# Kernel optimization log

Measured on AMD Instinct MI355X. Metric: run time of the kernel, lower is better.

The kernel has to match this reference:

```python
import jax, jax.numpy as jnp
import numpy as np


def setup_inputs() -> dict:
    key = jax.random.key(0)
    k0, k1, k2, k3 = jax.random.split(key, 4)
    B, in_dim, n_vars, out_dim, E = 64, 512, 512, 720, 8
    x = jax.random.normal(k0, (B, in_dim, n_vars), dtype=jnp.float32)
    # Gating: nn.Linear(in_dim, E, bias=False) -> weight [E, in_dim]
    Wg = jax.random.normal(k1, (E, in_dim), dtype=jnp.float32) * 0.02
    # Experts: nn.Linear(in_dim, out_dim) -> weight [out_dim, in_dim], bias [out_dim]
    We = jax.random.normal(k2, (E, out_dim, in_dim), dtype=jnp.float32) * 0.02
    be = jax.random.normal(k3, (E, out_dim), dtype=jnp.float32) * 0.02
    return {"x": x, "Wg": Wg, "We": We, "be": be, "top_k": 2}


def reference(x, Wg, We, be, top_k):
    # x: [B, in_len, n_vars] -> tokens along n_vars with feature dim in_len
    xt = jnp.swapaxes(x, 1, 2)                      # [B, V, D]
    gate = jax.nn.softmax(xt @ Wg.T, axis=-1)       # [B, V, E]
    weights, sel = jax.lax.top_k(gate, top_k)       # [B, V, k]
    E, O, D = We.shape
    out = jnp.zeros(xt.shape[:2] + (O,), dtype=xt.dtype)  # [B, V, O]
    for e in range(E):
        # combine weight for expert e: sum over top-k slots routed to e
        coef = jnp.sum(jnp.where(sel == e, weights, jnp.zeros_like(weights)), axis=-1)  # [B, V]
        out = out + coef[..., None] * (jnp.einsum('bvd,od->bvo', xt, We[e]) + be[e])
    return jnp.swapaxes(out, 1, 2)                  # [B, pred_len, n_vars]
```

## Files before the change

kernel.cpp:

```cpp
#include <hip/hip_runtime.h>
#include <hip/hip_bf16.h>

#define DID 512
#define NV  512
#define NB  64
#define OD  720
#define OPAD 768
#define NE  8
#define NTOK (NB * NV)
#define MAXTILE 512

typedef short  bf16x8 __attribute__((ext_vector_type(8)));
typedef float  f32x4  __attribute__((ext_vector_type(4)));

#define XT_OFF    0u
#define WB_OFF    33554432u
#define PID_OFF   39845888u
#define C1D_OFF   39976960u
#define C2D_OFF   40108032u
#define TL_OFF    40239104u
#define CL1_OFF   40370176u
#define CL2_OFF   40501248u
#define BCNT_OFF  40632320u
#define BFILL_OFF 40632576u
#define BOFF_OFF  40632832u
#define TPID_OFF  40633088u
#define TT0_OFF   40635136u
#define TEND_OFF  40637184u
#define NT_OFF    40639232u
#define SCR_OFF   40639488u
#define SCR_END   87825408u

static __device__ __forceinline__ ushort f2bf(float f) {
  unsigned u = __float_as_uint(f);
  unsigned r = (u + 0x7fffu + ((u >> 16) & 1u)) >> 16;
  return (ushort)r;
}
static __device__ __forceinline__ float bf2f(ushort u) {
  return __uint_as_float(((unsigned)u) << 16);
}
static __device__ __forceinline__ void async16(const ushort* g, ushort* l) {
  __builtin_amdgcn_global_load_lds((__attribute__((address_space(1))) void*)(g),
                                   (__attribute__((address_space(3))) void*)(l),
                                   16, 0, 0);
}
static __device__ __forceinline__ int swz(int r) { return (r & 3) ^ ((r >> 2) & 1); }

__global__ __launch_bounds__(256) void k_transpose(const float* __restrict__ x,
                                                   ushort* __restrict__ xt) {
  __shared__ float s[32][33];
  const int b  = blockIdx.z;
  const int v0 = blockIdx.x * 32;
  const int d0 = blockIdx.y * 32;
  const int tx = threadIdx.x & 31;
  const int ty = threadIdx.x >> 5;
  const float* xp = x + ((size_t)b * DID + d0 + ty) * NV + v0 + tx;
#pragma unroll
  for (int i = 0; i < 4; ++i) s[ty + i * 8][tx] = xp[(size_t)i * 8 * NV];
  __syncthreads();
#pragma unroll
  for (int i = 0; i < 4; ++i) {
    int vl = ty + i * 8;
    xt[((size_t)b * NV + v0 + vl) * DID + d0 + tx] = f2bf(s[tx][vl]);
  }
}

__global__ __launch_bounds__(256) void k_wbconv(const float* __restrict__ We,
                                                ushort* __restrict__ wb) {
  const int e = blockIdx.y;
  const int i = blockIdx.x * 256 + threadIdx.x;
  const int o = i >> 9;
  ushort val = 0;
  if (o < OD) val = f2bf(We[(size_t)e * OD * DID + i]);
  wb[(size_t)e * OPAD * DID + i] = val;
}

__global__ __launch_bounds__(256) void k_gate(const float* __restrict__ x,
                                              const float* __restrict__ Wg,
                                              int* __restrict__ pairid,
                                              float* __restrict__ c1d,
                                              float* __restrict__ c2d,
                                              int* __restrict__ bcnt) {
  __shared__ float wg[NE * DID];
  __shared__ int cnt64[64];
  const int tid = threadIdx.x;
  for (int i = tid; i < NE * DID; i += 256) wg[i] = Wg[i];
  if (tid < 64) cnt64[tid] = 0;
  __syncthreads();

  const int b = blockIdx.y;
  const int v = blockIdx.x * 256 + tid;
  const float* xp = x + (size_t)b * DID * NV + v;

  float acc[NE];
#pragma unroll
  for (int e = 0; e < NE; ++e) acc[e] = 0.f;
  for (int d = 0; d < DID; d += 4) {
    float x0 = xp[(size_t)(d + 0) * NV];
    float x1 = xp[(size_t)(d + 1) * NV];
    float x2 = xp[(size_t)(d + 2) * NV];
    float x3 = xp[(size_t)(d + 3) * NV];
#pragma unroll
    for (int e = 0; e < NE; ++e) {
      float4 w4 = *(const float4*)&wg[e * DID + d];
      acc[e] += x0 * w4.x + x1 * w4.y + x2 * w4.z + x3 * w4.w;
    }
  }
  float mx = acc[0];
#pragma unroll
  for (int e = 1; e < NE; ++e) mx = fmaxf(mx, acc[e]);
  float sum = 0.f;
#pragma unroll
  for (int e = 0; e < NE; ++e) { acc[e] = __expf(acc[e] - mx); sum += acc[e]; }
  const float inv = 1.f / sum;

  int i1 = 0; float g1 = acc[0];
#pragma unroll
  for (int e = 1; e < NE; ++e) if (acc[e] > g1) { g1 = acc[e]; i1 = e; }
  int i2 = -1; float g2 = -1.f;
#pragma unroll
  for (int e = 0; e < NE; ++e) if (e != i1 && acc[e] > g2) { g2 = acc[e]; i2 = e; }
  g1 *= inv; g2 *= inv;

  int ea, eb; float ca, cb;
  if (i1 < i2) { ea = i1; eb = i2; ca = g1; cb = g2; }
  else         { ea = i2; eb = i1; ca = g2; cb = g1; }
  const int pid = ea * 8 + eb;
  const int t = b * NV + v;
  pairid[t] = pid; c1d[t] = ca; c2d[t] = cb;
  atomicAdd(&cnt64[pid], 1);
  __syncthreads();
  if (tid < 64 && cnt64[tid]) atomicAdd(&bcnt[tid], cnt64[tid]);
}

__global__ void k_prefix(const int* __restrict__ bcnt, int* __restrict__ boffs,
                         int* __restrict__ tpid, int* __restrict__ tt0,
                         int* __restrict__ tend, int* __restrict__ ntp) {
  if (threadIdx.x != 0) return;
  int off = 0, nt = 0;
  for (int p = 0; p < 64; ++p) {
    boffs[p] = off;
    const int c = bcnt[p];
    const int end = off + c;
    for (int i = 0; i * 128 < c; ++i) {
      tpid[nt] = p; tt0[nt] = off + i * 128; tend[nt] = end; ++nt;
    }
    off = end;
  }
  ntp[0] = nt;
}

__global__ __launch_bounds__(256) void k_scatter(const int* __restrict__ pairid,
                                                 const float* __restrict__ c1d,
                                                 const float* __restrict__ c2d,
                                                 const int* __restrict__ boffs,
                                                 int* __restrict__ bfill,
                                                 int* __restrict__ tlist,
                                                 float* __restrict__ cl1,
                                                 float* __restrict__ cl2) {
  __shared__ int cnt64[64], base64[64];
  const int tid = threadIdx.x;
  if (tid < 64) cnt64[tid] = 0;
  __syncthreads();
  const int t = blockIdx.x * 256 + tid;
  const int pid = pairid[t];
  const int p = atomicAdd(&cnt64[pid], 1);
  __syncthreads();
  if (tid < 64) base64[tid] = cnt64[tid] ? atomicAdd(&bfill[tid], cnt64[tid]) : 0;
  __syncthreads();
  const int slot = boffs[pid] + base64[pid] + p;
  tlist[slot] = t; cl1[slot] = c1d[t]; cl2[slot] = c2d[t];
}

__global__ __launch_bounds__(256, 2) void k_gemm(
    const ushort* __restrict__ xt, const ushort* __restrict__ wb,
    const float* __restrict__ be, const int* __restrict__ tlist,
    const float* __restrict__ cl1, const float* __restrict__ cl2,
    const int* __restrict__ tpid, const int* __restrict__ tt0,
    const int* __restrict__ tendarr, const int* __restrict__ ntp,
    ushort* __restrict__ scratch, float* __restrict__ out, int mode) {
  const int tile = blockIdx.x;
  if (tile >= ntp[0]) return;
  const int pid  = tpid[tile];
  const int t0   = tt0[tile];
  const int tend = tendarr[tile];
  const int e1 = pid >> 3, e2 = pid & 7;
  const int o0 = blockIdx.y * 128;

  __shared__ __align__(16) ushort As[2][4096];
  __shared__ __align__(16) ushort Bs[2][4096];

  const int tid  = threadIdx.x;
  const int lane = tid & 63;
  const int w    = tid >> 6;

  const int f0 = w * 128 + lane, f1 = f0 + 64;
  const int r0 = f0 >> 2, p0 = f0 & 3, q0 = p0 ^ swz(r0);
  const int r1 = f1 >> 2, p1 = f1 & 3, q1 = p1 ^ swz(r1);

  const int aoff0 = (o0 + r0) * DID + q0 * 8;
  const int aoff1 = (o0 + r1) * DID + q1 * 8;
  const int sl0 = t0 + r0, sl1 = t0 + r1;
  const int tok0 = (sl0 < tend) ? tlist[sl0] : 0;
  const int tok1 = (sl1 < tend) ? tlist[sl1] : 0;
  const int boff0 = tok0 * DID + q0 * 8;
  const int boff1 = tok1 * DID + q1 * 8;
  const int dA0 = w * 1024, dA1 = w * 1024 + 512;

  const int m    = lane & 15;
  const int quad = lane >> 4;
  const int wo   = (w >> 1) * 64;
  const int wt   = (w & 1) * 64;

  f32x4 acc[4][4];
#pragma unroll
  for (int i = 0; i < 4; ++i)
#pragma unroll
    for (int j = 0; j < 4; ++j) acc[i][j] = (f32x4){0.f, 0.f, 0.f, 0.f};

  {
    const ushort* wA = wb + (size_t)e1 * OPAD * DID;
    async16(wA + aoff0, &As[0][dA0]);
    async16(wA + aoff1, &As[0][dA1]);
    async16(xt + boff0, &Bs[0][dA0]);
    async16(xt + boff1, &Bs[0][dA1]);
  }

  for (int kk = 0; kk < 32; ++kk) {
    __syncthreads();

    if (kk == 16) {
      float ratio[4];
#pragma unroll
      for (int j = 0; j < 4; ++j) {
        const int sl = t0 + wt + j * 16 + m;
        const bool g = sl < tend;
        const float cc1 = g ? cl1[sl] : 0.f;
        const float cc2 = g ? cl2[sl] : 1.f;
        ratio[j] = cc1 / cc2;
      }
      const float* be1p = be + e1 * OD;
#pragma unroll
      for (int i = 0; i < 4; ++i) {
        const int ob = o0 + wo + i * 16 + quad * 4;
        float b0 = 0, b1 = 0, b2 = 0, b3 = 0;
        if (ob < OD) { b0 = be1p[ob]; b1 = be1p[ob + 1]; b2 = be1p[ob + 2]; b3 = be1p[ob + 3]; }
#pragma unroll
        for (int j = 0; j < 4; ++j) {
          acc[i][j][0] = (acc[i][j][0] + b0) * ratio[j];
          acc[i][j][1] = (acc[i][j][1] + b1) * ratio[j];
          acc[i][j][2] = (acc[i][j][2] + b2) * ratio[j];
          acc[i][j][3] = (acc[i][j][3] + b3) * ratio[j];
        }
      }
    }

    const int nk = kk + 1;
    if (nk < 32) {
      const int nb = nk & 1;
      const int eA = (nk < 16) ? e1 : e2;
      const int k0 = (nk & 15) * 32;
      const ushort* wA = wb + (size_t)eA * OPAD * DID + k0;
      async16(wA + aoff0, &As[nb][dA0]);
      async16(wA + aoff1, &As[nb][dA1]);
      async16(xt + boff0 + k0, &Bs[nb][dA0]);
      async16(xt + boff1 + k0, &Bs[nb][dA1]);
    }

    const int cb = kk & 1;
    bf16x8 af[4], bfr[4];
#pragma unroll
    for (int i = 0; i < 4; ++i) {
      const int R = wo + i * 16 + m;
      af[i] = *(const bf16x8*)(&As[cb][R * 32 + ((quad ^ swz(R)) << 3)]);
    }
#pragma unroll
    for (int j = 0; j < 4; ++j) {
      const int R = wt + j * 16 + m;
      bfr[j] = *(const bf16x8*)(&Bs[cb][R * 32 + ((quad ^ swz(R)) << 3)]);
    }
#pragma unroll
    for (int i = 0; i < 4; ++i)
#pragma unroll
      for (int j = 0; j < 4; ++j)
        acc[i][j] = __builtin_amdgcn_mfma_f32_16x16x32_bf16(af[i], bfr[j],
                                                            acc[i][j], 0, 0, 0);
  }

  float c2v[4]; int tokv[4]; bool gv[4];
#pragma unroll
  for (int j = 0; j < 4; ++j) {
    const int sl = t0 + wt + j * 16 + m;
    gv[j] = sl < tend;
    c2v[j]  = gv[j] ? cl2[sl] : 0.f;
    tokv[j] = gv[j] ? tlist[sl] : 0;
  }
  const float* be2p = be + e2 * OD;
#pragma unroll
  for (int i = 0; i < 4; ++i) {
    const int ob = o0 + wo + i * 16 + quad * 4;
    if (ob < OD) {
      const float b0 = be2p[ob], b1 = be2p[ob + 1], b2 = be2p[ob + 2], b3 = be2p[ob + 3];
#pragma unroll
      for (int j = 0; j < 4; ++j) {
        if (gv[j]) {
          const float v0 = c2v[j] * (acc[i][j][0] + b0);
          const float v1 = c2v[j] * (acc[i][j][1] + b1);
          const float v2 = c2v[j] * (acc[i][j][2] + b2);
          const float v3 = c2v[j] * (acc[i][j][3] + b3);
          if (mode == 0) {
            ushort4 pk = make_ushort4(f2bf(v0), f2bf(v1), f2bf(v2), f2bf(v3));
            *(ushort4*)(scratch + (size_t)tokv[j] * OD + ob) = pk;
          } else {
            const int bb = tokv[j] >> 9, vv = tokv[j] & 511;
            float* op = out + ((size_t)bb * OD + ob) * NV + vv;
            op[0] = v0; op[(size_t)NV] = v1; op[2 * (size_t)NV] = v2; op[3 * (size_t)NV] = v3;
          }
        }
      }
    }
  }
}

__global__ __launch_bounds__(256) void k_combine(const ushort* __restrict__ scratch,
                                                 float* __restrict__ out) {
  __shared__ ushort s[64][68];
  const int v0 = blockIdx.x * 64;
  const int o0 = blockIdx.y * 64;
  const int b  = blockIdx.z;
  const int tid = threadIdx.x;
#pragma unroll
  for (int it = 0; it < 2; ++it) {
    const int c = it * 256 + tid;
    const int row = c >> 3, cg = c & 7;
    const int o = o0 + cg * 8;
    if (o + 8 <= OD) {
      const ushort* src = scratch + ((size_t)(b * NV + v0 + row)) * OD + o;
      ushort4 ua = *(const ushort4*)(src);
      ushort4 ub = *(const ushort4*)(src + 4);
      *(ushort4*)&s[row][cg * 8] = ua;
      *(ushort4*)&s[row][cg * 8 + 4] = ub;
    }
  }
  __syncthreads();
  const int vv = tid & 63;
  const int og = tid >> 6;
#pragma unroll
  for (int oi = 0; oi < 8; ++oi) {
    const int ol = (og * 8 + oi) * 2;
    const int o = o0 + ol;
    if (o < OD) {
      ushort2 u = *(const ushort2*)&s[vv][ol];
      float* op = out + ((size_t)b * OD + o) * NV + v0 + vv;
      op[0]  = bf2f(u.x);
      op[NV] = bf2f(u.y);
    }
  }
}

extern "C" void kernel_launch(void* const* d_in, const int* in_sizes, int n_in,
                              void* d_out, int out_size, void* d_ws, size_t ws_size,
                              hipStream_t stream) {
  const float* x  = (const float*)d_in[0];
  const float* Wg = (const float*)d_in[1];
  const float* We = (const float*)d_in[2];
  const float* be = (const float*)d_in[3];
  float* out = (float*)d_out;

  char* ws = (char*)d_ws;
  ushort* xt     = (ushort*)(ws + XT_OFF);
  ushort* wb     = (ushort*)(ws + WB_OFF);
  int*    pairid = (int*)   (ws + PID_OFF);
  float*  c1d    = (float*) (ws + C1D_OFF);
  float*  c2d    = (float*) (ws + C2D_OFF);
  int*    tlist  = (int*)   (ws + TL_OFF);
  float*  cl1    = (float*) (ws + CL1_OFF);
  float*  cl2    = (float*) (ws + CL2_OFF);
  int*    bcnt   = (int*)   (ws + BCNT_OFF);
  int*    bfill  = (int*)   (ws + BFILL_OFF);
  int*    boffs  = (int*)   (ws + BOFF_OFF);
  int*    tpid   = (int*)   (ws + TPID_OFF);
  int*    tt0    = (int*)   (ws + TT0_OFF);
  int*    tend   = (int*)   (ws + TEND_OFF);
  int*    ntp    = (int*)   (ws + NT_OFF);
  ushort* scratch= (ushort*)(ws + SCR_OFF);

  const int mode = (ws_size >= (size_t)SCR_END) ? 0 : 1;

  (void)hipMemsetAsync(bcnt, 0, 512, stream);

  k_transpose<<<dim3(NV / 32, DID / 32, NB), 256, 0, stream>>>(x, xt);
  k_wbconv<<<dim3(OPAD * DID / 256, NE), 256, 0, stream>>>(We, wb);
  k_gate<<<dim3(NV / 256, NB), 256, 0, stream>>>(x, Wg, pairid, c1d, c2d, bcnt);
  k_prefix<<<1, 64, 0, stream>>>(bcnt, boffs, tpid, tt0, tend, ntp);
  k_scatter<<<NTOK / 256, 256, 0, stream>>>(pairid, c1d, c2d, boffs, bfill,
                                            tlist, cl1, cl2);
  k_gemm<<<dim3(320, OPAD / 128), 256, 0, stream>>>(xt, wb, be, tlist, cl1, cl2,
                                                    tpid, tt0, tend, ntp,
                                                    scratch, out, mode);
  if (mode == 0)
    k_combine<<<dim3(NV / 64, (OD + 63) / 64, NB), 256, 0, stream>>>(scratch, out);
}
```

Baseline: 341.0 us.

## Fuse transpose/bf16 conversion into gating kernel and parallelize prefix scan

Merges the separate transpose-to-bf16 kernel and the gating kernel into one kernel, so x (64 MB fp32) is read from global memory once instead of twice. Each block handles 64 tokens with 8 waves splitting the feature dimension, then reduces partial gate logits in shared memory before softmax/top-2. Also replaces the single-thread serial prefix over expert pairs with a 64-lane wavefront shuffle scan. The trade-off is more shared memory per block and fewer, larger blocks. The transposed writes are now 16-byte per-lane stores strided by the row length, which may coalesce less well than the old LDS-tiled transpose.

Measured after the change: 322.1 us. 5.5% less time.

```diff
diff --git a/kernel.cpp b/kernel.cpp
--- a/kernel.cpp
+++ b/kernel.cpp
@@ -46,23 +46,92 @@
 }
 static __device__ __forceinline__ int swz(int r) { return (r & 3) ^ ((r >> 2) & 1); }
 
-__global__ __launch_bounds__(256) void k_transpose(const float* __restrict__ x,
-                                                   ushort* __restrict__ xt) {
-  __shared__ float s[32][33];
-  const int b  = blockIdx.z;
-  const int v0 = blockIdx.x * 32;
-  const int d0 = blockIdx.y * 32;
-  const int tx = threadIdx.x & 31;
-  const int ty = threadIdx.x >> 5;
-  const float* xp = x + ((size_t)b * DID + d0 + ty) * NV + v0 + tx;
-#pragma unroll
-  for (int i = 0; i < 4; ++i) s[ty + i * 8][tx] = xp[(size_t)i * 8 * NV];
-  __syncthreads();
-#pragma unroll
-  for (int i = 0; i < 4; ++i) {
-    int vl = ty + i * 8;
-    xt[((size_t)b * NV + v0 + vl) * DID + d0 + tx] = f2bf(s[tx][vl]);
-  }
+__global__ __launch_bounds__(512) void k_gatet(const float* __restrict__ x,
+                                               const float* __restrict__ Wg,
+                                               ushort* __restrict__ xt,
+                                               int* __restrict__ pairid,
+                                               float* __restrict__ c1d,
+                                               float* __restrict__ c2d,
+                                               int* __restrict__ bcnt) {
+  __shared__ float wg[NE * DID];
+  __shared__ float part[8][64][NE + 1];
+  __shared__ int cnt64[64];
+  const int tid = threadIdx.x;
+  for (int i = tid; i < NE * DID / 4; i += 512)
+    ((float4*)wg)[i] = ((const float4*)Wg)[i];
+  if (tid < 64) cnt64[tid] = 0;
+  __syncthreads();
+
+  const int b    = blockIdx.y;
+  const int v0   = blockIdx.x * 64;
+  const int w    = tid >> 6;
+  const int lane = tid & 63;
+  const int v    = v0 + lane;
+  const int d0   = w * 64;
+  const float* xp = x + ((size_t)b * DID + d0) * NV + v;
+  ushort* xtp = xt + ((size_t)b * NV + v) * DID + d0;
+
+  float acc[NE];
+#pragma unroll
+  for (int e = 0; e < NE; ++e) acc[e] = 0.f;
+
+  for (int c = 0; c < 64; c += 8) {
+    float xv[8];
+#pragma unroll
+    for (int u = 0; u < 8; ++u) xv[u] = xp[(size_t)(c + u) * NV];
+#pragma unroll
+    for (int e = 0; e < NE; ++e) {
+      const float* wp = &wg[e * DID + d0 + c];
+      float4 wa = *(const float4*)wp;
+      float4 wb4 = *(const float4*)(wp + 4);
+      acc[e] += xv[0] * wa.x + xv[1] * wa.y + xv[2] * wa.z + xv[3] * wa.w
+              + xv[4] * wb4.x + xv[5] * wb4.y + xv[6] * wb4.z + xv[7] * wb4.w;
+    }
+    bf16x8 pk;
+#pragma unroll
+    for (int u = 0; u < 8; ++u) pk[u] = (short)f2bf(xv[u]);
+    *(bf16x8*)(xtp + c) = pk;
+  }
+
+#pragma unroll
+  for (int e = 0; e < NE; ++e) part[w][lane][e] = acc[e];
+  __syncthreads();
+
+  if (tid < 64) {
+    float a[NE];
+#pragma unroll
+    for (int e = 0; e < NE; ++e) {
+      float s = part[0][tid][e];
+#pragma unroll
+      for (int q = 1; q < 8; ++q) s += part[q][tid][e];
+      a[e] = s;
+    }
+    float mx = a[0];
+#pragma unroll
+    for (int e = 1; e < NE; ++e) mx = fmaxf(mx, a[e]);
+    float sum = 0.f;
+#pragma unroll
+    for (int e = 0; e < NE; ++e) { a[e] = __expf(a[e] - mx); sum += a[e]; }
+    const float inv = 1.f / sum;
+
+    int i1 = 0; float g1 = a[0];
+#pragma unroll
+    for (int e = 1; e < NE; ++e) if (a[e] > g1) { g1 = a[e]; i1 = e; }
+    int i2 = -1; float g2 = -1.f;
+#pragma unroll
+    for (int e = 0; e < NE; ++e) if (e != i1 && a[e] > g2) { g2 = a[e]; i2 = e; }
+    g1 *= inv; g2 *= inv;
+
+    int ea, eb; float ca, cb;
+    if (i1 < i2) { ea = i1; eb = i2; ca = g1; cb = g2; }
+    else         { ea = i2; eb = i1; ca = g2; cb = g1; }
+    const int pid = ea * 8 + eb;
+    const int t = b * NV + v0 + tid;
+    pairid[t] = pid; c1d[t] = ca; c2d[t] = cb;
+    atomicAdd(&cnt64[pid], 1);
+  }
+  __syncthreads();
+  if (tid < 64 && cnt64[tid]) atomicAdd(&bcnt[tid], cnt64[tid]);
 }
 
 __global__ __launch_bounds__(256) void k_wbconv(const float* __restrict__ We,
@@ -75,79 +144,33 @@
   wb[(size_t)e * OPAD * DID + i] = val;
 }
 
-__global__ __launch_bounds__(256) void k_gate(const float* __restrict__ x,
-                                              const float* __restrict__ Wg,
-                                              int* __restrict__ pairid,
-                                              float* __restrict__ c1d,
-                                              float* __restrict__ c2d,
-                                              int* __restrict__ bcnt) {
-  __shared__ float wg[NE * DID];
-  __shared__ int cnt64[64];
-  const int tid = threadIdx.x;
-  for (int i = tid; i < NE * DID; i += 256) wg[i] = Wg[i];
-  if (tid < 64) cnt64[tid] = 0;
-  __syncthreads();
-
-  const int b = blockIdx.y;
-  const int v = blockIdx.x * 256 + tid;
-  const float* xp = x + (size_t)b * DID * NV + v;
-
-  float acc[NE];
-#pragma unroll
-  for (int e = 0; e < NE; ++e) acc[e] = 0.f;
-  for (int d = 0; d < DID; d += 4) {
-    float x0 = xp[(size_t)(d + 0) * NV];
-    float x1 = xp[(size_t)(d + 1) * NV];
-    float x2 = xp[(size_t)(d + 2) * NV];
-    float x3 = xp[(size_t)(d + 3) * NV];
-#pragma unroll
-    for (int e = 0; e < NE; ++e) {
-      float4 w4 = *(const float4*)&wg[e * DID + d];
-      acc[e] += x0 * w4.x + x1 * w4.y + x2 * w4.z + x3 * w4.w;
-    }
-  }
-  float mx = acc[0];
-#pragma unroll
-  for (int e = 1; e < NE; ++e) mx = fmaxf(mx, acc[e]);
-  float sum = 0.f;
-#pragma unroll
-  for (int e = 0; e < NE; ++e) { acc[e] = __expf(acc[e] - mx); sum += acc[e]; }
-  const float inv = 1.f / sum;
-
-  int i1 = 0; float g1 = acc[0];
-#pragma unroll
-  for (int e = 1; e < NE; ++e) if (acc[e] > g1) { g1 = acc[e]; i1 = e; }
-  int i2 = -1; float g2 = -1.f;
-#pragma unroll
-  for (int e = 0; e < NE; ++e) if (e != i1 && acc[e] > g2) { g2 = acc[e]; i2 = e; }
-  g1 *= inv; g2 *= inv;
-
-  int ea, eb; float ca, cb;
-  if (i1 < i2) { ea = i1; eb = i2; ca = g1; cb = g2; }
-  else         { ea = i2; eb = i1; ca = g2; cb = g1; }
-  const int pid = ea * 8 + eb;
-  const int t = b * NV + v;
-  pairid[t] = pid; c1d[t] = ca; c2d[t] = cb;
-  atomicAdd(&cnt64[pid], 1);
-  __syncthreads();
-  if (tid < 64 && cnt64[tid]) atomicAdd(&bcnt[tid], cnt64[tid]);
-}
-
 __global__ void k_prefix(const int* __restrict__ bcnt, int* __restrict__ boffs,
                          int* __restrict__ tpid, int* __restrict__ tt0,
                          int* __restrict__ tend, int* __restrict__ ntp) {
-  if (threadIdx.x != 0) return;
-  int off = 0, nt = 0;
-  for (int p = 0; p < 64; ++p) {
-    boffs[p] = off;
-    const int c = bcnt[p];
-    const int end = off + c;
-    for (int i = 0; i * 128 < c; ++i) {
-      tpid[nt] = p; tt0[nt] = off + i * 128; tend[nt] = end; ++nt;
-    }
-    off = end;
-  }
-  ntp[0] = nt;
+  const int p = threadIdx.x;
+  const int c = bcnt[p];
+  int run = c;
+#pragma unroll
+  for (int s = 1; s < 64; s <<= 1) {
+    int up = __shfl_up(run, s, 64);
+    if (p >= s) run += up;
+  }
+  const int excl = run - c;
+  boffs[p] = excl;
+  const int ntiles = (c + 127) >> 7;
+  int trun = ntiles;
+#pragma unroll
+  for (int s = 1; s < 64; s <<= 1) {
+    int up = __shfl_up(trun, s, 64);
+    if (p >= s) trun += up;
+  }
+  const int texcl = trun - ntiles;
+  for (int i = 0; i < ntiles; ++i) {
+    tpid[texcl + i] = p;
+    tt0[texcl + i]  = excl + i * 128;
+    tend[texcl + i] = excl + c;
+  }
+  if (p == 63) ntp[0] = texcl + ntiles;
 }
 
 __global__ __launch_bounds__(256) void k_scatter(const int* __restrict__ pairid,
@@ -389,9 +412,8 @@
 
   (void)hipMemsetAsync(bcnt, 0, 512, stream);
 
-  k_transpose<<<dim3(NV / 32, DID / 32, NB), 256, 0, stream>>>(x, xt);
+  k_gatet<<<dim3(NV / 64, NB), 512, 0, stream>>>(x, Wg, xt, pairid, c1d, c2d, bcnt);
   k_wbconv<<<dim3(OPAD * DID / 256, NE), 256, 0, stream>>>(We, wb);
-  k_gate<<<dim3(NV / 256, NB), 256, 0, stream>>>(x, Wg, pairid, c1d, c2d, bcnt);
   k_prefix<<<1, 64, 0, stream>>>(bcnt, boffs, tpid, tt0, tend, ntp);
   k_scatter<<<NTOK / 256, 256, 0, stream>>>(pairid, c1d, c2d, boffs, bfill,
                                             tlist, cl1, cl2);
```
